# Kernel tuning notes

Measured on AMD Instinct MI355X. Metric: run time of the kernel, lower is better.

Reference implementation:

```python
import jax, jax.numpy as jnp
import numpy as np

DIM = 64
HEADS = 8
DIM_HEAD = 64
INNER = HEADS * DIM_HEAD  # 512
MLP = 256
DEPTH = 4
B = 64
HW = 15
NPATCH = HW * HW  # 225
N = NPATCH + 1    # 226 tokens incl cls
SCALE = DIM_HEAD ** -0.5
EPS = 1e-5


def setup_inputs() -> dict:
    key = jax.random.key(0)
    ks = jax.random.split(key, 20)
    s = 0.02
    inp = {
        "hsi": jax.random.normal(ks[0], (B, DIM, HW, HW), jnp.float32),
        "lidar": jax.random.normal(ks[1], (B, DIM, HW, HW), jnp.float32),
        "cls_hsi": jax.random.normal(ks[2], (1, 1, DIM), jnp.float32),
        "cls_lidar": jax.random.normal(ks[3], (1, 1, DIM), jnp.float32),
        "pos_hsi": jax.random.normal(ks[4], (1, N, DIM), jnp.float32),
        "pos_lidar": jax.random.normal(ks[5], (1, N, DIM), jnp.float32),
        "fmg_w": jax.random.normal(ks[6], (2 * DIM, DIM * DIM), jnp.float32) * s,
        "ln1_g": jnp.ones((DEPTH, DIM), jnp.float32),
        "ln1_b": jnp.zeros((DEPTH, DIM), jnp.float32),
        "qkv_w": jax.random.normal(ks[7], (DEPTH, DIM, 3 * INNER), jnp.float32) * s,
        "out_w": jax.random.normal(ks[8], (DEPTH, INNER, DIM), jnp.float32) * s,
        "out_b": jnp.zeros((DEPTH, DIM), jnp.float32),
        "ln2_g": jnp.ones((DEPTH, DIM), jnp.float32),
        "ln2_b": jnp.zeros((DEPTH, DIM), jnp.float32),
        "ff_w1": jax.random.normal(ks[9], (DEPTH, DIM, MLP), jnp.float32) * s,
        "ff_b1": jnp.zeros((DEPTH, MLP), jnp.float32),
        "ff_w2": jax.random.normal(ks[10], (DEPTH, MLP, DIM), jnp.float32) * s,
        "ff_b2": jnp.zeros((DEPTH, DIM), jnp.float32),
    }
    return inp


def _ln(x, g, b):
    m = x.mean(-1, keepdims=True)
    v = ((x - m) ** 2).mean(-1, keepdims=True)
    return (x - m) * jax.lax.rsqrt(v + EPS) * g + b


def _attn(x, dfm, g, b, wqkv, wo, bo):
    # x: [B, N, DIM]; dfm: [B, DIM_HEAD] diagonal of per-sample fusion matrix
    xn = _ln(x, g, b)
    qkv = xn @ wqkv  # [B, N, 3*INNER]
    q, k, v = jnp.split(qkv, 3, axis=-1)
    def heads(t):
        return t.reshape(B, N, HEADS, DIM_HEAD).transpose(0, 2, 1, 3)  # bhnd
    q, v = heads(q), heads(v)
    # torch.einsum('bhnd,bdd->bhnd', q, fm): repeated 'd' in bdd = diagonal of fm
    k = q * dfm[:, None, None, :]
    dots = jnp.einsum('bhid,bhjd->bhij', q, k) * SCALE
    attn = jax.nn.softmax(dots, axis=-1)
    out = jnp.einsum('bhij,bhjd->bhid', attn, v)
    out = out.transpose(0, 2, 1, 3).reshape(B, N, INNER)
    return out @ wo + bo


def _ff(x, g, b, w1, b1, w2, b2):
    xn = _ln(x, g, b)
    h = jax.nn.gelu(xn @ w1 + b1, approximate=False)
    return h @ w2 + b2


def reference(hsi, lidar, cls_hsi, cls_lidar, pos_hsi, pos_lidar, fmg_w,
              ln1_g, ln1_b, qkv_w, out_w, out_b, ln2_g, ln2_b,
              ff_w1, ff_b1, ff_w2, ff_b2):
    # patch_to_embedding with p1=p2=1: b c h w -> b (h w) c
    h_e = hsi.reshape(B, DIM, NPATCH).transpose(0, 2, 1)
    l_e = lidar.reshape(B, DIM, NPATCH).transpose(0, 2, 1)

    # fusion matrix from pre-exchange embeddings
    x = jnp.concatenate([h_e.mean(1), l_e.mean(1)], axis=-1)  # [B, 2*DIM]
    fm = jax.nn.sigmoid(x @ fmg_w).reshape(B, DIM, DIM)
    dfm = jnp.diagonal(fm, axis1=1, axis2=2)  # [B, DIM]

    # _exchange_embedding (faithful to source: reads both halves from hsi)
    n2 = NPATCH // 2
    h_ex = jnp.concatenate([h_e[:, :n2], h_e[:, n2:]], axis=1)
    l_ex = jnp.concatenate([h_e[:, :n2], h_e[:, n2:]], axis=1)

    h_ex = jnp.concatenate([jnp.broadcast_to(cls_hsi, (B, 1, DIM)), h_ex], axis=1)
    l_ex = jnp.concatenate([jnp.broadcast_to(cls_lidar, (B, 1, DIM)), l_ex], axis=1)
    h_ex = h_ex + pos_hsi[:, :N]
    l_ex = l_ex + pos_lidar[:, :N]

    def run_layers(h, l):
        for i in range(DEPTH):
            h = _attn(h, dfm, ln1_g[i], ln1_b[i], qkv_w[i], out_w[i], out_b[i]) + h
            h = _ff(h, ln2_g[i], ln2_b[i], ff_w1[i], ff_b1[i], ff_w2[i], ff_b2[i]) + h
            l = _attn(l, dfm, ln1_g[i], ln1_b[i], qkv_w[i], out_w[i], out_b[i]) + l
            l = _ff(l, ln2_g[i], ln2_b[i], ff_w1[i], ff_b1[i], ff_w2[i], ff_b2[i]) + l
        return h, l

    h_ex, l_ex = run_layers(h_ex, l_ex)

    # _exchange_token: swap cls tokens
    h_new = jnp.concatenate([l_ex[:, :1], h_ex[:, 1:]], axis=1)
    l_new = jnp.concatenate([h_ex[:, :1], l_ex[:, 1:]], axis=1)

    h_new, l_new = run_layers(h_new, l_new)
    return h_new[:, 0] + l_new[:, 0]
```

## Files before the change

kernel.cpp:

```cpp
#include <hip/hip_runtime.h>
#include <hip/hip_bf16.h>
#include <cstdint>

#define NB 64
#define ND 64
#define NH 8
#define DH 64
#define NIN 512
#define NMLP 256
#define NDEPTH 4
#define NPATCH 225
#define NTOK 226
#define NSB 128
#define NROWS (NSB*NTOK)

#define VP 240

typedef __attribute__((ext_vector_type(8))) short bfrag8;
typedef __attribute__((ext_vector_type(4))) float ffrag4;

__device__ __forceinline__ unsigned short f2b(float f) {
  uint32_t u; __builtin_memcpy(&u, &f, 4);
  u += 0x7fff + ((u >> 16) & 1);
  return (unsigned short)(u >> 16);
}

__global__ void k_dfm(const float* __restrict__ hsi, const float* __restrict__ lidar,
                      const float* __restrict__ fmg_w, float* __restrict__ sdfm) {
  __shared__ float xc[128];
  int b = blockIdx.x, t = threadIdx.x;
  const float* src = (t < 64) ? hsi : lidar;
  int d = t & 63;
  const float* p = src + ((size_t)b * 64 + d) * NPATCH;
  float s = 0.f;
  for (int i = 0; i < NPATCH; ++i) s += p[i];
  xc[t] = s * (1.0f / 225.0f);
  __syncthreads();
  if (t < 64) {
    float acc = 0.f;
    const float* w = fmg_w + t * 65;
    for (int c = 0; c < 128; ++c) acc += xc[c] * w[c * 4096];
    float sg = 1.0f / (1.0f + expf(-acc));
    sdfm[b * 64 + t] = sqrtf(sg);
  }
}

__global__ void k_build(const float* __restrict__ hsi,
                        const float* __restrict__ cls_h, const float* __restrict__ cls_l,
                        const float* __restrict__ pos_h, const float* __restrict__ pos_l,
                        const float* __restrict__ g, const float* __restrict__ bb,
                        float* __restrict__ X, uint16_t* __restrict__ Xn) {
  int r = blockIdx.x;
  int sb = r / NTOK, n = r - sb * NTOK;
  int s = sb >> 6, b = sb & 63;
  int d = threadIdx.x;
  float v;
  if (n == 0) v = s ? cls_l[d] : cls_h[d];
  else        v = hsi[((size_t)b * 64 + d) * NPATCH + (n - 1)];
  v += (s ? pos_l : pos_h)[n * ND + d];
  X[(size_t)r * ND + d] = v;
  float sm = v, sq = v * v;
  #pragma unroll
  for (int o = 32; o; o >>= 1) { sm += __shfl_xor(sm, o); sq += __shfl_xor(sq, o); }
  float m = sm * (1.f / 64.f);
  float rs = rsqrtf(sq * (1.f / 64.f) - m * m + 1e-5f);
  Xn[(size_t)r * ND + d] = f2b((v - m) * rs * g[d] + bb[d]);
}

__global__ __launch_bounds__(256) void k_wconv(
    const float* __restrict__ qkv_w, const float* __restrict__ out_w,
    const float* __restrict__ ff_w1, const float* __restrict__ ff_w2,
    uint16_t* __restrict__ Wqv, uint16_t* __restrict__ Wo,
    uint16_t* __restrict__ W1, uint16_t* __restrict__ W2) {
  int i = blockIdx.x * 256 + threadIdx.x;
  if (i < 262144) {
    int ly = i >> 16, rem = i & 65535, n = rem >> 6, k = rem & 63;
    int col = n + ((n >> 9) << 9);
    Wqv[i] = f2b(qkv_w[((size_t)ly * 64 + k) * 1536 + col]);
  } else if (i < 393216) {
    int j = i - 262144;
    int ly = j >> 15, rem = j & 32767, n = rem >> 9, k = rem & 511;
    Wo[j] = f2b(out_w[((size_t)ly * 512 + k) * 64 + n]);
  } else if (i < 458752) {
    int j = i - 393216;
    int ly = j >> 14, rem = j & 16383, n = rem >> 6, k = rem & 63;
    W1[j] = f2b(ff_w1[((size_t)ly * 64 + k) * 256 + n]);
  } else {
    int j = i - 458752;
    int ly = j >> 14, rem = j & 16383, n = rem >> 8, k = rem & 255;
    W2[j] = f2b(ff_w2[((size_t)ly * 256 + k) * 64 + n]);
  }
}

__global__ __launch_bounds__(512) void k_fattn(const uint16_t* __restrict__ Xn,
    const uint16_t* __restrict__ Wqv,
    const float* __restrict__ sdfm, uint16_t* __restrict__ Og) {
  __shared__ __align__(16) uint16_t qs[240 * 64];
  __shared__ __align__(16) uint16_t vt[64 * VP];
  __shared__ __align__(16) uint16_t pb[8][512];
  int bh = blockIdx.x;
  int sb = bh >> 3, h = bh & 7;
  int t = threadIdx.x, w = t >> 6, l = t & 63;
  int quad = l >> 4, c = l & 15;
  const uint16_t* Xb = Xn + (size_t)sb * NTOK * ND;

  float sf[4];
  #pragma unroll
  for (int dt = 0; dt < 4; ++dt)
    sf[dt] = sdfm[(sb & 63) * 64 + dt * 16 + c] * 0.35355339059327373f;

  for (int it = w; it < 15; it += 8) {
    int i0 = it * 16;
    int ri = i0 + c; if (ri > 225) ri = 225;
    bfrag8 a0 = *(const bfrag8*)(Xb + (size_t)ri * 64 + quad * 8);
    bfrag8 a1 = *(const bfrag8*)(Xb + (size_t)ri * 64 + 32 + quad * 8);
    #pragma unroll
    for (int dt = 0; dt < 4; ++dt) {
      int nq = h * 64 + dt * 16 + c;
      bfrag8 bq0 = *(const bfrag8*)(Wqv + (size_t)nq * 64 + quad * 8);
      bfrag8 bq1 = *(const bfrag8*)(Wqv + (size_t)nq * 64 + 32 + quad * 8);
      ffrag4 zq = {0.f, 0.f, 0.f, 0.f};
      zq = __builtin_amdgcn_mfma_f32_16x16x32_bf16(a0, bq0, zq, 0, 0, 0);
      zq = __builtin_amdgcn_mfma_f32_16x16x32_bf16(a1, bq1, zq, 0, 0, 0);
      bfrag8 bv0 = *(const bfrag8*)(Wqv + (size_t)(512 + nq) * 64 + quad * 8);
      bfrag8 bv1 = *(const bfrag8*)(Wqv + (size_t)(512 + nq) * 64 + 32 + quad * 8);
      ffrag4 zv = {0.f, 0.f, 0.f, 0.f};
      zv = __builtin_amdgcn_mfma_f32_16x16x32_bf16(a0, bv0, zv, 0, 0, 0);
      zv = __builtin_amdgcn_mfma_f32_16x16x32_bf16(a1, bv1, zv, 0, 0, 0);
      int d = dt * 16 + c;
      #pragma unroll
      for (int r = 0; r < 4; ++r) {
        int i = i0 + quad * 4 + r;
        qs[i * 64 + ((((d >> 3) ^ (i & 7))) << 3) + (d & 7)] = f2b(zq[r] * sf[dt]);
        vt[d * VP + i] = f2b(zv[r]);
      }
    }
  }
  __syncthreads();

  uint16_t* pw = &pb[w][0];
  for (int it = w; it < 15; it += 8) {
    int i0 = it * 16;
    int ra = i0 + c, sa = ra & 7;
    bfrag8 a0 = *(const bfrag8*)(qs + ra * 64 + ((quad ^ sa) << 3));
    bfrag8 a1 = *(const bfrag8*)(qs + ra * 64 + (((quad + 4) ^ sa) << 3));
    ffrag4 acc[15];
    #pragma unroll
    for (int jt = 0; jt < 15; ++jt) {
      int rb = jt * 16 + c, sk = rb & 7;
      bfrag8 b0 = *(const bfrag8*)(qs + rb * 64 + ((quad ^ sk) << 3));
      bfrag8 b1 = *(const bfrag8*)(qs + rb * 64 + (((quad + 4) ^ sk) << 3));
      ffrag4 z = {0.f, 0.f, 0.f, 0.f};
      z = __builtin_amdgcn_mfma_f32_16x16x32_bf16(a0, b0, z, 0, 0, 0);
      z = __builtin_amdgcn_mfma_f32_16x16x32_bf16(a1, b1, z, 0, 0, 0);
      acc[jt] = z;
    }
    float rinv[4];
    #pragma unroll
    for (int r = 0; r < 4; ++r) {
      float m = -1e30f;
      #pragma unroll
      for (int jt = 0; jt < 15; ++jt) m = fmaxf(m, acc[jt][r]);
      #pragma unroll
      for (int o = 8; o; o >>= 1) m = fmaxf(m, __shfl_xor(m, o));
      float s = 0.f;
      #pragma unroll
      for (int jt = 0; jt < 15; ++jt) {
        float p = __expf(acc[jt][r] - m);
        if (jt == 14 && c >= 2) p = 0.f;
        acc[jt][r] = p;
        s += p;
      }
      #pragma unroll
      for (int o = 8; o; o >>= 1) s += __shfl_xor(s, o);
      rinv[r] = 1.f / s;
    }
    ffrag4 oa[4];
    #pragma unroll
    for (int dt = 0; dt < 4; ++dt) oa[dt] = (ffrag4){0.f, 0.f, 0.f, 0.f};
    for (int jc = 0; jc < 8; ++jc) {
      if (jc == 7) {
        *(uint64_t*)(pw + c * 32 + 16 + quad * 4) = 0ull;
      }
      #pragma unroll
      for (int r = 0; r < 4; ++r) {
        int row = quad * 4 + r;
        pw[row * 32 + c] = f2b(acc[2 * jc][r]);
        if (jc < 7) pw[row * 32 + 16 + c] = f2b(acc[2 * jc + 1][r]);
      }
      bfrag8 pa = *(const bfrag8*)(pw + c * 32 + quad * 8);
      int j0 = jc * 32;
      #pragma unroll
      for (int dt = 0; dt < 4; ++dt) {
        bfrag8 vb;
        if (jc < 7)
          vb = *(const bfrag8*)(vt + (dt * 16 + c) * VP + j0 + quad * 8);
        else
          vb = *(const bfrag8*)(vt + (dt * 16 + c) * VP + 224 + (quad & 1) * 8);
        oa[dt] = __builtin_amdgcn_mfma_f32_16x16x32_bf16(pa, vb, oa[dt], 0, 0, 0);
      }
    }
    #pragma unroll
    for (int dt = 0; dt < 4; ++dt) {
      #pragma unroll
      for (int r = 0; r < 4; ++r) {
        int i = i0 + quad * 4 + r;
        if (i < NTOK)
          Og[((size_t)sb * NTOK + i) * NIN + h * DH + dt * 16 + c] =
              f2b(oa[dt][r] * rinv[r]);
      }
    }
  }
}

__global__ __launch_bounds__(64) void k_pf(const uint16_t* __restrict__ Og,
    const uint16_t* __restrict__ Wot,
    const float* __restrict__ bo, float* __restrict__ X,
    const float* __restrict__ g2, const float* __restrict__ bb2,
    const uint16_t* __restrict__ W1t,
    const float* __restrict__ b1,
    const uint16_t* __restrict__ W2t,
    const float* __restrict__ b2,
    const float* __restrict__ gn, const float* __restrict__ bbn,
    uint16_t* __restrict__ XnOut) {
  __shared__ __align__(16) uint16_t xa2[16 * 72];
  __shared__ __align__(16) uint16_t ha[16 * 264];
  int t = threadIdx.x;
  int quad = t >> 4, c = t & 15;
  int r0 = blockIdx.x * 16;

  const uint16_t* orow = Og + (size_t)(r0 + c) * 512 + quad * 8;
  bfrag8 a[16];
  #pragma unroll
  for (int kc = 0; kc < 16; ++kc) a[kc] = *(const bfrag8*)(orow + kc * 32);
  ffrag4 acc[4];
  #pragma unroll
  for (int jt = 0; jt < 4; ++jt) acc[jt] = (ffrag4){0.f, 0.f, 0.f, 0.f};
  #pragma unroll
  for (int kc = 0; kc < 16; ++kc) {
    #pragma unroll
    for (int jt = 0; jt < 4; ++jt) {
      bfrag8 b = *(const bfrag8*)(Wot + (size_t)(jt * 16 + c) * 512 + kc * 32 + quad * 8);
      acc[jt] = __builtin_amdgcn_mfma_f32_16x16x32_bf16(a[kc], b, acc[jt], 0, 0, 0);
    }
  }
  float xv[4][4];
  #pragma unroll
  for (int jt = 0; jt < 4; ++jt) {
    float bv = bo[jt * 16 + c];
    #pragma unroll
    for (int r = 0; r < 4; ++r) {
      int il = quad * 4 + r;
      size_t idx = (size_t)(r0 + il) * 64 + jt * 16 + c;
      float v = X[idx] + acc[jt][r] + bv;
      X[idx] = v;
      xv[jt][r] = v;
    }
  }
  #pragma unroll
  for (int r = 0; r < 4; ++r) {
    float s = xv[0][r] + xv[1][r] + xv[2][r] + xv[3][r];
    float q = xv[0][r]*xv[0][r] + xv[1][r]*xv[1][r] + xv[2][r]*xv[2][r] + xv[3][r]*xv[3][r];
    #pragma unroll
    for (int o = 8; o; o >>= 1) { s += __shfl_xor(s, o); q += __shfl_xor(q, o); }
    float m = s * (1.f / 64.f);
    float rs = rsqrtf(q * (1.f / 64.f) - m * m + 1e-5f);
    int il = quad * 4 + r;
    #pragma unroll
    for (int jt = 0; jt < 4; ++jt) {
      int n = jt * 16 + c;
      xa2[il * 72 + n] = f2b((xv[jt][r] - m) * rs * g2[n] + bb2[n]);
    }
  }
  const uint16_t* xrow = xa2 + c * 72;
  bfrag8 a0 = *(const bfrag8*)(xrow + quad * 8);
  bfrag8 a1 = *(const bfrag8*)(xrow + 32 + quad * 8);
  ffrag4 acc1[16];
  #pragma unroll
  for (int jt = 0; jt < 16; ++jt) {
    bfrag8 b0  = *(const bfrag8*)(W1t + (size_t)(jt * 16 + c) * 64 + quad * 8);
    bfrag8 b1f = *(const bfrag8*)(W1t + (size_t)(jt * 16 + c) * 64 + 32 + quad * 8);
    ffrag4 z = {0.f, 0.f, 0.f, 0.f};
    z = __builtin_amdgcn_mfma_f32_16x16x32_bf16(a0, b0, z, 0, 0, 0);
    z = __builtin_amdgcn_mfma_f32_16x16x32_bf16(a1, b1f, z, 0, 0, 0);
    acc1[jt] = z;
  }
  #pragma unroll
  for (int jt = 0; jt < 16; ++jt) {
    float bv = b1[jt * 16 + c];
    #pragma unroll
    for (int r = 0; r < 4; ++r) {
      float z = acc1[jt][r] + bv;
      float hg = 0.5f * z * (1.f + erff(z * 0.7071067811865476f));
      ha[(quad * 4 + r) * 264 + jt * 16 + c] = f2b(hg);
    }
  }
  ffrag4 o2[4];
  #pragma unroll
  for (int jt = 0; jt < 4; ++jt) o2[jt] = (ffrag4){0.f, 0.f, 0.f, 0.f};
  #pragma unroll
  for (int kc = 0; kc < 8; ++kc) {
    bfrag8 pa = *(const bfrag8*)(ha + c * 264 + kc * 32 + quad * 8);
    #pragma unroll
    for (int jt = 0; jt < 4; ++jt) {
      bfrag8 vb = *(const bfrag8*)(W2t + (size_t)(jt * 16 + c) * 256 + kc * 32 + quad * 8);
      o2[jt] = __builtin_amdgcn_mfma_f32_16x16x32_bf16(pa, vb, o2[jt], 0, 0, 0);
    }
  }
  float yv[4][4];
  #pragma unroll
  for (int jt = 0; jt < 4; ++jt) {
    float bv = b2[jt * 16 + c];
    #pragma unroll
    for (int r = 0; r < 4; ++r) {
      int il = quad * 4 + r;
      size_t idx = (size_t)(r0 + il) * 64 + jt * 16 + c;
      float v = X[idx] + o2[jt][r] + bv;
      X[idx] = v;
      yv[jt][r] = v;
    }
  }
  #pragma unroll
  for (int r = 0; r < 4; ++r) {
    float s = yv[0][r] + yv[1][r] + yv[2][r] + yv[3][r];
    float q = yv[0][r]*yv[0][r] + yv[1][r]*yv[1][r] + yv[2][r]*yv[2][r] + yv[3][r]*yv[3][r];
    #pragma unroll
    for (int o = 8; o; o >>= 1) { s += __shfl_xor(s, o); q += __shfl_xor(q, o); }
    float m = s * (1.f / 64.f);
    float rs = rsqrtf(q * (1.f / 64.f) - m * m + 1e-5f);
    int il = quad * 4 + r;
    #pragma unroll
    for (int jt = 0; jt < 4; ++jt) {
      int n = jt * 16 + c;
      XnOut[(size_t)(r0 + il) * 64 + n] = f2b((yv[jt][r] - m) * rs * gn[n] + bbn[n]);
    }
  }
}

__global__ void k_xchg(float* __restrict__ X, uint16_t* __restrict__ Xn,
                       const float* __restrict__ g, const float* __restrict__ bb) {
  int b = blockIdx.x, d = threadIdx.x;
  size_t i0 = (size_t)(b * NTOK) * ND + d;
  size_t i1 = (size_t)((64 + b) * NTOK) * ND + d;
  float a = X[i0], cc = X[i1];
  X[i0] = cc; X[i1] = a;
  float s0 = cc, q0 = cc * cc, s1 = a, q1 = a * a;
  #pragma unroll
  for (int o = 32; o; o >>= 1) {
    s0 += __shfl_xor(s0, o); q0 += __shfl_xor(q0, o);
    s1 += __shfl_xor(s1, o); q1 += __shfl_xor(q1, o);
  }
  float m0 = s0 * (1.f / 64.f), rs0 = rsqrtf(q0 * (1.f / 64.f) - m0 * m0 + 1e-5f);
  float m1 = s1 * (1.f / 64.f), rs1 = rsqrtf(q1 * (1.f / 64.f) - m1 * m1 + 1e-5f);
  Xn[i0] = f2b((cc - m0) * rs0 * g[d] + bb[d]);
  Xn[i1] = f2b((a - m1) * rs1 * g[d] + bb[d]);
}

__global__ void k_out(const float* __restrict__ X, float* __restrict__ out) {
  int i = blockIdx.x * 64 + threadIdx.x;
  int b = i >> 6, d = i & 63;
  out[i] = X[(size_t)b * NTOK * ND + d] + X[(size_t)(64 + b) * NTOK * ND + d];
}

extern "C" void kernel_launch(void* const* d_in, const int* in_sizes, int n_in,
                              void* d_out, int out_size, void* d_ws, size_t ws_size,
                              hipStream_t stream) {
  const float* hsi   = (const float*)d_in[0];
  const float* lidar = (const float*)d_in[1];
  const float* cls_h = (const float*)d_in[2];
  const float* cls_l = (const float*)d_in[3];
  const float* pos_h = (const float*)d_in[4];
  const float* pos_l = (const float*)d_in[5];
  const float* fmg_w = (const float*)d_in[6];
  const float* ln1_g = (const float*)d_in[7];
  const float* ln1_b = (const float*)d_in[8];
  const float* qkv_w = (const float*)d_in[9];
  const float* out_w = (const float*)d_in[10];
  const float* out_b = (const float*)d_in[11];
  const float* ln2_g = (const float*)d_in[12];
  const float* ln2_b = (const float*)d_in[13];
  const float* ff_w1 = (const float*)d_in[14];
  const float* ff_b1 = (const float*)d_in[15];
  const float* ff_w2 = (const float*)d_in[16];
  const float* ff_b2 = (const float*)d_in[17];

  char* ws = (char*)d_ws;
  float*    X    = (float*)ws;
  float*    sdfm = (float*)(ws + 7405568);
  uint16_t* Xn   = (uint16_t*)(ws + 7421952);
  uint16_t* Og   = (uint16_t*)(ws + 11124736);
  uint16_t* Wqv  = (uint16_t*)(ws + 40747008);
  uint16_t* Wo   = (uint16_t*)(ws + 41271296);
  uint16_t* W1   = (uint16_t*)(ws + 41533440);
  uint16_t* W2   = (uint16_t*)(ws + 41664512);

  k_wconv<<<2048, 256, 0, stream>>>(qkv_w, out_w, ff_w1, ff_w2, Wqv, Wo, W1, W2);
  k_dfm<<<NB, 128, 0, stream>>>(hsi, lidar, fmg_w, sdfm);
  k_build<<<NROWS, 64, 0, stream>>>(hsi, cls_h, cls_l, pos_h, pos_l,
                                    ln1_g, ln1_b, X, Xn);
  for (int pass = 0; pass < 2; ++pass) {
    for (int ly = 0; ly < NDEPTH; ++ly) {
      int nx = (ly + 1) & 3;
      k_fattn<<<NSB * NH, 512, 0, stream>>>(Xn, Wqv + (size_t)ly * 65536, sdfm, Og);
      k_pf<<<NROWS / 16, 64, 0, stream>>>(Og, Wo + (size_t)ly * 32768, out_b + ly * ND,
                                          X, ln2_g + ly * ND, ln2_b + ly * ND,
                                          W1 + (size_t)ly * 16384, ff_b1 + ly * NMLP,
                                          W2 + (size_t)ly * 16384, ff_b2 + ly * ND,
                                          ln1_g + nx * ND, ln1_b + nx * ND, Xn);
    }
    if (pass == 0) k_xchg<<<64, 64, 0, stream>>>(X, Xn, ln1_g, ln1_b);
  }
  k_out<<<64, 64, 0, stream>>>(X, (float*)d_out);
}
```

Before: 811.4 us.

## Compute transposed scores and build P fragments in registers via permlane swaps

```diff
diff --git a/kernel.cpp b/kernel.cpp
--- a/kernel.cpp
+++ b/kernel.cpp
@@ -14,7 +14,7 @@
 #define NSB 128
 #define NROWS (NSB*NTOK)
 
-#define VP 240
+#define VP 232
 
 typedef __attribute__((ext_vector_type(8))) short bfrag8;
 typedef __attribute__((ext_vector_type(4))) float ffrag4;
@@ -23,6 +23,12 @@
   uint32_t u; __builtin_memcpy(&u, &f, 4);
   u += 0x7fff + ((u >> 16) & 1);
   return (unsigned short)(u >> 16);
+}
+
+__device__ __forceinline__ unsigned pk2(float lo, float hi) {
+  unsigned r;
+  asm("v_cvt_pk_bf16_f32 %0, %1, %2" : "=v"(r) : "v"(lo), "v"(hi));
+  return r;
 }
 
 __global__ void k_dfm(const float* __restrict__ hsi, const float* __restrict__ lidar,
@@ -92,17 +98,18 @@
   }
 }
 
-__global__ __launch_bounds__(512) void k_fattn(const uint16_t* __restrict__ Xn,
+__global__ __launch_bounds__(512, 4) void k_fattn(const uint16_t* __restrict__ Xn,
     const uint16_t* __restrict__ Wqv,
     const float* __restrict__ sdfm, uint16_t* __restrict__ Og) {
   __shared__ __align__(16) uint16_t qs[240 * 64];
-  __shared__ __align__(16) uint16_t vt[64 * VP];
-  __shared__ __align__(16) uint16_t pb[8][512];
+  __shared__ __align__(16) uint16_t vt[64 * VP + 32];
   int bh = blockIdx.x;
   int sb = bh >> 3, h = bh & 7;
   int t = threadIdx.x, w = t >> 6, l = t & 63;
   int quad = l >> 4, c = l & 15;
   const uint16_t* Xb = Xn + (size_t)sb * NTOK * ND;
+
+  if (t < 32) vt[64 * VP + t] = 0;
 
   float sf[4];
   #pragma unroll
@@ -132,74 +139,91 @@
       for (int r = 0; r < 4; ++r) {
         int i = i0 + quad * 4 + r;
         qs[i * 64 + ((((d >> 3) ^ (i & 7))) << 3) + (d & 7)] = f2b(zq[r] * sf[dt]);
-        vt[d * VP + i] = f2b(zv[r]);
+      }
+      int iv = i0 + quad * 4;
+      if (iv + 3 < VP) {
+        unsigned lo = pk2(zv[0], zv[1]);
+        unsigned hi = pk2(zv[2], zv[3]);
+        *(unsigned long long*)(vt + (size_t)d * VP + iv) =
+            ((unsigned long long)hi << 32) | lo;
       }
     }
   }
   __syncthreads();
 
-  uint16_t* pw = &pb[w][0];
   for (int it = w; it < 15; it += 8) {
     int i0 = it * 16;
-    int ra = i0 + c, sa = ra & 7;
-    bfrag8 a0 = *(const bfrag8*)(qs + ra * 64 + ((quad ^ sa) << 3));
-    bfrag8 a1 = *(const bfrag8*)(qs + ra * 64 + (((quad + 4) ^ sa) << 3));
+    int rb = i0 + c, sk = rb & 7;
+    bfrag8 b0 = *(const bfrag8*)(qs + rb * 64 + ((quad ^ sk) << 3));
+    bfrag8 b1 = *(const bfrag8*)(qs + rb * 64 + (((quad + 4) ^ sk) << 3));
     ffrag4 acc[15];
     #pragma unroll
     for (int jt = 0; jt < 15; ++jt) {
-      int rb = jt * 16 + c, sk = rb & 7;
-      bfrag8 b0 = *(const bfrag8*)(qs + rb * 64 + ((quad ^ sk) << 3));
-      bfrag8 b1 = *(const bfrag8*)(qs + rb * 64 + (((quad + 4) ^ sk) << 3));
+      int ra = jt * 16 + c, sa = ra & 7;
+      bfrag8 a0 = *(const bfrag8*)(qs + ra * 64 + ((quad ^ sa) << 3));
+      bfrag8 a1 = *(const bfrag8*)(qs + ra * 64 + (((quad + 4) ^ sa) << 3));
       ffrag4 z = {0.f, 0.f, 0.f, 0.f};
       z = __builtin_amdgcn_mfma_f32_16x16x32_bf16(a0, b0, z, 0, 0, 0);
       z = __builtin_amdgcn_mfma_f32_16x16x32_bf16(a1, b1, z, 0, 0, 0);
       acc[jt] = z;
     }
-    float rinv[4];
-    #pragma unroll
-    for (int r = 0; r < 4; ++r) {
-      float m = -1e30f;
+    #pragma unroll
+    for (int r = 0; r < 4; ++r)
+      if (quad * 4 + r >= 2) acc[14][r] = -1e30f;
+    float m = -1e30f;
+    #pragma unroll
+    for (int jt = 0; jt < 15; ++jt)
       #pragma unroll
-      for (int jt = 0; jt < 15; ++jt) m = fmaxf(m, acc[jt][r]);
-      #pragma unroll
-      for (int o = 8; o; o >>= 1) m = fmaxf(m, __shfl_xor(m, o));
-      float s = 0.f;
-      #pragma unroll
-      for (int jt = 0; jt < 15; ++jt) {
-        float p = __expf(acc[jt][r] - m);
-        if (jt == 14 && c >= 2) p = 0.f;
-        acc[jt][r] = p;
-        s += p;
-      }
-      #pragma unroll
-      for (int o = 8; o; o >>= 1) s += __shfl_xor(s, o);
-      rinv[r] = 1.f / s;
-    }
-    ffrag4 oa[4];
-    #pragma unroll
-    for (int dt = 0; dt < 4; ++dt) oa[dt] = (ffrag4){0.f, 0.f, 0.f, 0.f};
-    for (int jc = 0; jc < 8; ++jc) {
-      if (jc == 7) {
-        *(uint64_t*)(pw + c * 32 + 16 + quad * 4) = 0ull;
-      }
+      for (int r = 0; r < 4; ++r) m = fmaxf(m, acc[jt][r]);
+    m = fmaxf(m, __shfl_xor(m, 16));
+    m = fmaxf(m, __shfl_xor(m, 32));
+    float s = 0.f;
+    #pragma unroll
+    for (int jt = 0; jt < 15; ++jt)
       #pragma unroll
       for (int r = 0; r < 4; ++r) {
-        int row = quad * 4 + r;
-        pw[row * 32 + c] = f2b(acc[2 * jc][r]);
-        if (jc < 7) pw[row * 32 + 16 + c] = f2b(acc[2 * jc + 1][r]);
-      }
-      bfrag8 pa = *(const bfrag8*)(pw + c * 32 + quad * 8);
-      int j0 = jc * 32;
+        float e = __expf(acc[jt][r] - m);
+        acc[jt][r] = e;
+        s += e;
+      }
+    s += __shfl_xor(s, 16);
+    s += __shfl_xor(s, 32);
+    float rinv = 1.f / s;
+
+    ffrag4 oa[4];
+    #pragma unroll
+    for (int dt = 0; dt < 4; ++dt) oa[dt] = (ffrag4){0.f, 0.f, 0.f, 0.f};
+
+    #pragma unroll
+    for (int jj = 0; jj < 8; ++jj) {
+      unsigned XA0 = pk2(acc[2 * jj][0], acc[2 * jj][1]);
+      unsigned XA1 = pk2(acc[2 * jj][2], acc[2 * jj][3]);
+      unsigned XB0 = 0, XB1 = 0;
+      if (jj < 7) {
+        XB0 = pk2(acc[2 * jj + 1][0], acc[2 * jj + 1][1]);
+        XB1 = pk2(acc[2 * jj + 1][2], acc[2 * jj + 1][3]);
+      }
+      unsigned Pa = XA0, Qa = XB0, Pb = XA1, Qb = XB1;
+      asm("v_permlane32_swap_b32 %0, %1" : "+v"(Pa), "+v"(Qa));
+      asm("v_permlane32_swap_b32 %0, %1" : "+v"(Pb), "+v"(Qb));
+      unsigned P0s = __shfl_xor(Pa, 16), Q0s = __shfl_xor(Qa, 16);
+      unsigned P1s = __shfl_xor(Pb, 16), Q1s = __shfl_xor(Qb, 16);
+      bool qlo = (quad & 1) == 0;
+      union { unsigned u[4]; bfrag8 f; } pu;
+      pu.u[0] = qlo ? Pa  : Q0s;
+      pu.u[1] = qlo ? Pb  : Q1s;
+      pu.u[2] = qlo ? P0s : Qa;
+      pu.u[3] = qlo ? P1s : Qb;
+      int j0 = jj * 32;
       #pragma unroll
       for (int dt = 0; dt < 4; ++dt) {
-        bfrag8 vb;
-        if (jc < 7)
-          vb = *(const bfrag8*)(vt + (dt * 16 + c) * VP + j0 + quad * 8);
-        else
-          vb = *(const bfrag8*)(vt + (dt * 16 + c) * VP + 224 + (quad & 1) * 8);
-        oa[dt] = __builtin_amdgcn_mfma_f32_16x16x32_bf16(pa, vb, oa[dt], 0, 0, 0);
-      }
-    }
+        bfrag8 vb = *(const bfrag8*)(vt + (dt * 16 + c) * VP + j0 + quad * 8);
+        oa[dt] = __builtin_amdgcn_mfma_f32_16x16x32_bf16(pu.f, vb, oa[dt], 0, 0, 0);
+      }
+    }
+    float rr[4];
+    #pragma unroll
+    for (int r = 0; r < 4; ++r) rr[r] = __shfl(rinv, quad * 4 + r);
     #pragma unroll
     for (int dt = 0; dt < 4; ++dt) {
       #pragma unroll
@@ -207,7 +231,7 @@
         int i = i0 + quad * 4 + r;
         if (i < NTOK)
           Og[((size_t)sb * NTOK + i) * NIN + h * DH + dt * 16 + c] =
-              f2b(oa[dt][r] * rinv[r]);
+              f2b(oa[dt][r] * rr[r]);
       }
     }
   }
```

New measurement: 1.375 ms. +69.5%, slower.
